# Kernel tuning notes

Measured on AMD Instinct MI355X. Metric: run time of the kernel, lower is better.

The kernel has to match this reference:

```python
import jax, jax.numpy as jnp
import numpy as np

B, K, D = 8, 4000, 256
H, DQ, DV = 8, 32, 32
WIN, PAD = 200, 50
STEP = WIN - 2 * PAD  # 100
BETA = 0.25


def setup_inputs() -> dict:
    key = jax.random.key(0)
    ks = jax.random.split(key, 14)
    s = 0.02
    return {
        "query": jax.random.normal(ks[0], (B, K, D), jnp.float32),
        "key": jax.random.normal(ks[1], (B, K, D), jnp.float32),
        "value": jax.random.normal(ks[2], (B, K, D), jnp.float32),
        "Wq": jax.random.normal(ks[3], (D, H * DQ), jnp.float32) * s,
        "bq": jax.random.normal(ks[4], (H * DQ,), jnp.float32) * s,
        "Wk": jax.random.normal(ks[5], (D, H * DQ), jnp.float32) * s,
        "bk": jax.random.normal(ks[6], (H * DQ,), jnp.float32) * s,
        "Wv": jax.random.normal(ks[7], (D, H * DV), jnp.float32) * s,
        "bv": jax.random.normal(ks[8], (H * DV,), jnp.float32) * s,
        "Wo": jax.random.normal(ks[9], (H * DV, D), jnp.float32) * s,
        "bo": jax.random.normal(ks[10], (D,), jnp.float32) * s,
    }


def _windows(x, n_win):
    starts = jnp.arange(n_win) * STEP
    idx = starts[:, None] + jnp.arange(WIN)[None, :]
    return x[:, :, idx, :]


def reference(query, key, value, Wq, bq, Wk, bk, Wv, bv, Wo, bo):
    b, k_len, d = query.shape
    pad = lambda t: jnp.pad(t, ((0, 0), (PAD, PAD), (0, 0)), mode='edge')  # replicate pad
    qp, kp, vp = pad(query), pad(key), pad(value)
    kpad = k_len + 2 * PAD
    n_win = (kpad - WIN) // STEP + 1

    def proj(x, Wm, bias, dh):
        y = x @ Wm + bias                       # [B, Kp, H*dh]
        return y.reshape(b, kpad, H, dh).transpose(0, 2, 1, 3)  # [B, H, Kp, dh]

    q = _windows(proj(qp, Wq, bq, DQ), n_win)
    kk = _windows(proj(kp, Wk, bk, DQ), n_win)
    v = _windows(proj(vp, Wv, bv, DV), n_win)

    scores = jnp.einsum('bhnid,bhnjd->bhnij', q, kk) / jnp.sqrt(jnp.float32(WIN))
    dist = jnp.abs(jnp.arange(WIN)[:, None] - jnp.arange(WIN)[None, :]).astype(scores.dtype)
    cauchy = (1.0 / (1.0 + BETA * dist * dist)) * (1.0 - jnp.eye(WIN, dtype=scores.dtype))
    scores = scores * cauchy
    causal = jnp.triu(jnp.ones((WIN, WIN), dtype=bool), k=1)  # attention_size is not None -> causal masking
    scores = jnp.where(causal, -jnp.inf, scores)
    attn = jax.nn.softmax(scores, axis=-1)
    out = jnp.einsum('bhnij,bhnjd->bhnid', attn, v)
    out = out[:, :, :, PAD:WIN - PAD, :].reshape(b, H, k_len, DV)
    out = out.transpose(0, 2, 1, 3).reshape(b, k_len, H * DV)  # heads concatenated, head-major slices
    return out @ Wo + bo
```

## Files before the change

kernel.cpp:

```cpp
#include <hip/hip_runtime.h>


typedef __bf16 bf16_t;
typedef __bf16 bf16x8 __attribute__((ext_vector_type(8)));
typedef float  f32x4  __attribute__((ext_vector_type(4)));

#define MFMA16(a, b, c) __builtin_amdgcn_mfma_f32_16x16x32_bf16((a), (b), (c), 0, 0, 0)

static __device__ __forceinline__ bf16x8 cvt8(float4 a, float4 b) {
  bf16x8 r;
  r[0] = (bf16_t)a.x; r[1] = (bf16_t)a.y; r[2] = (bf16_t)a.z; r[3] = (bf16_t)a.w;
  r[4] = (bf16_t)b.x; r[5] = (bf16_t)b.y; r[6] = (bf16_t)b.z; r[7] = (bf16_t)b.w;
  return r;
}

static __device__ __forceinline__ unsigned short bbits(bf16_t v) {
  union { bf16_t b; unsigned short u; } c; c.b = v; return c.u;
}

__global__ __launch_bounds__(256)
void prep_weights(const float* __restrict__ Wq, const float* __restrict__ Wk,
                  const float* __restrict__ Wv, const float* __restrict__ Wo,
                  bf16_t* __restrict__ wt) {
  const int mat  = blockIdx.x >> 6;
  const int tile = blockIdx.x & 63;
  const int kt = (tile >> 3) * 32, nt = (tile & 7) * 32;
  const float* W = (mat == 0) ? Wq : (mat == 1) ? Wk : (mat == 2) ? Wv : Wo;
  __shared__ float t[32][33];
  const int tx = threadIdx.x & 31, ty = threadIdx.x >> 5;
#pragma unroll
  for (int i = 0; i < 32; i += 8)
    t[ty + i][tx] = W[(size_t)(kt + ty + i) * 256 + nt + tx];
  __syncthreads();
  bf16_t* dst = wt + (size_t)mat * 65536;
#pragma unroll
  for (int i = 0; i < 32; i += 8)
    dst[(size_t)(nt + ty + i) * 256 + kt + tx] = (bf16_t)t[tx][ty + i];
}

static __device__ __forceinline__ void stage_B(const bf16_t* __restrict__ W,
                                               bf16_t* lb, int tid) {
#pragma unroll
  for (int i = 0; i < 16; ++i) {
    const int g    = tid + i * 512;
    const int row  = g >> 5;
    const int colb = (g & 31) << 4;
    const bf16x8 w = *(const bf16x8*)&W[row * 256 + (colb >> 1)];
    *(bf16x8*)((char*)lb + row * 512 + (colb ^ ((row & 7) << 4))) = w;
  }
}

__global__ __launch_bounds__(512)
void proj_gemm(const float* __restrict__ qx, const float* __restrict__ kx,
               const float* __restrict__ vx, const bf16_t* __restrict__ wt,
               const float* __restrict__ bq, const float* __restrict__ bk,
               const float* __restrict__ bv,
               bf16_t* __restrict__ qb, bf16_t* __restrict__ kb,
               bf16_t* __restrict__ vt, int M, float qscale) {
  const int mode = blockIdx.y;
  const float* X    = (mode == 0) ? qx : (mode == 1) ? kx : vx;
  const float* bias = (mode == 0) ? bq : (mode == 1) ? bk : bv;

  __shared__ bf16_t lb[65536];
  const int tid = threadIdx.x;
  stage_B(wt + (size_t)mode * 65536, lb, tid);

  const int lane = tid & 63, wv = tid >> 6;
  const int lo = lane & 15, hi = lane >> 4;
  const int m0 = blockIdx.x * 128;
  int ar = m0 + wv * 16 + lo; if (ar >= M) ar = M - 1;

  bf16x8 areg[8];
#pragma unroll
  for (int kk = 0; kk < 8; ++kk) {
    const float* ap = X + (size_t)ar * 256 + kk * 32 + hi * 8;
    areg[kk] = cvt8(((const float4*)ap)[0], ((const float4*)ap)[1]);
  }
  __syncthreads();

  f32x4 acc[16] = {};
#pragma unroll
  for (int kk = 0; kk < 8; ++kk) {
#pragma unroll
    for (int ni = 0; ni < 16; ++ni) {
      const int row = ni * 16 + lo;
      const int off = row * 512 + (((kk * 64) + hi * 16) ^ ((row & 7) << 4));
      const bf16x8 bfrag = *(const bf16x8*)((const char*)lb + off);
      acc[ni] = MFMA16(areg[kk], bfrag, acc[ni]);
    }
  }

  const int mb = m0 + wv * 16 + hi * 4;
  if (mb >= M) return;
#pragma unroll
  for (int ni = 0; ni < 16; ++ni) {
    const int n = ni * 16 + lo;
    const float bia = bias[n];
    if (mode == 0) {
#pragma unroll
      for (int r = 0; r < 4; ++r)
        qb[(size_t)(mb + r) * 256 + n] = (bf16_t)((acc[ni][r] + bia) * qscale);
    } else if (mode == 1) {
      const int b = mb / 4000, t = mb - b * 4000;
#pragma unroll
      for (int r = 0; r < 4; ++r)
        kb[((size_t)b * 4064 + t + 50 + r) * 256 + n] = (bf16_t)(acc[ni][r] + bia);
    } else {
      const int b = mb / 4000, t = mb - b * 4000;
      const int h = n >> 5, dv = n & 31;
      bf16_t* O = vt + ((size_t)((b * 8 + h) * 32 + dv)) * 4064 + t + 50;
      unsigned short e0 = bbits((bf16_t)(acc[ni][0] + bia));
      unsigned short e1 = bbits((bf16_t)(acc[ni][1] + bia));
      unsigned short e2 = bbits((bf16_t)(acc[ni][2] + bia));
      unsigned short e3 = bbits((bf16_t)(acc[ni][3] + bia));
      unsigned* O32 = (unsigned*)O;
      O32[0] = (unsigned)e0 | ((unsigned)e1 << 16);
      O32[1] = (unsigned)e2 | ((unsigned)e3 << 16);
    }
  }
}

__global__ __launch_bounds__(512)
void out_gemm(const bf16_t* __restrict__ ao, const bf16_t* __restrict__ wt,
              const float* __restrict__ bias, float* __restrict__ Out, int M) {
  __shared__ bf16_t lb[65536];
  const int tid = threadIdx.x;
  stage_B(wt, lb, tid);

  const int lane = tid & 63, wv = tid >> 6;
  const int lo = lane & 15, hi = lane >> 4;
  const int m0 = blockIdx.x * 128;
  int ar = m0 + wv * 16 + lo; if (ar >= M) ar = M - 1;

  bf16x8 areg[8];
#pragma unroll
  for (int kk = 0; kk < 8; ++kk)
    areg[kk] = *(const bf16x8*)&ao[(size_t)ar * 256 + kk * 32 + hi * 8];
  __syncthreads();

  f32x4 acc[16] = {};
#pragma unroll
  for (int kk = 0; kk < 8; ++kk) {
#pragma unroll
    for (int ni = 0; ni < 16; ++ni) {
      const int row = ni * 16 + lo;
      const int off = row * 512 + (((kk * 64) + hi * 16) ^ ((row & 7) << 4));
      const bf16x8 bfrag = *(const bf16x8*)((const char*)lb + off);
      acc[ni] = MFMA16(areg[kk], bfrag, acc[ni]);
    }
  }

  const int mb = m0 + wv * 16 + hi * 4;
  if (mb >= M) return;
#pragma unroll
  for (int ni = 0; ni < 16; ++ni) {
    const int n = ni * 16 + lo;
    const float bia = bias[n];
#pragma unroll
    for (int r = 0; r < 4; ++r)
      Out[(size_t)(mb + r) * 256 + n] = acc[ni][r] + bia;
  }
}

__global__ void fill_edges(bf16_t* __restrict__ kb, bf16_t* __restrict__ vt, int nb) {
  const int idx = blockIdx.x * 256 + threadIdx.x;
  const int kcnt = nb * 64 * 256;
  if (idx < kcnt) {
    const int b  = idx >> 14;
    const int pp = (idx >> 8) & 63;
    const int nn = idx & 255;
    const int p  = (pp < 50) ? pp : pp + 4000;
    bf16_t v = (pp < 50) ? kb[((size_t)b * 4064 + 50) * 256 + nn] : (bf16_t)0.f;
    kb[((size_t)b * 4064 + p) * 256 + nn] = v;
  } else {
    const int j  = idx - kcnt;
    const int bh = j >> 11;
    const int dv = (j >> 6) & 31;
    const int pp = j & 63;
    const int p  = (pp < 50) ? pp : pp + 4000;
    bf16_t v = (pp < 50) ? vt[((size_t)bh * 32 + dv) * 4064 + 50] : (bf16_t)0.f;
    vt[((size_t)bh * 32 + dv) * 4064 + p] = v;
  }
}

__global__ __launch_bounds__(448)
void attn_win(const bf16_t* __restrict__ qb, const bf16_t* __restrict__ kb,
              const bf16_t* __restrict__ vt, bf16_t* __restrict__ ao) {
  const int blk = blockIdx.x;
  const int n = blk % 40;
  const int h = (blk / 40) & 7;
  const int b = blk / 320;
  const int wv = threadIdx.x >> 6;
  const int lane = threadIdx.x & 63;
  const int lo = lane & 15, hi = lane >> 4;

  __shared__ __align__(16) bf16_t E[7][16][40];

  const int i0 = 50 + 16 * wv;
  int jtmax = (65 + 16 * wv) >> 4;
  if (jtmax > 9) jtmax = 9;
  const int reach = jtmax * 16 + 16;

  int tq = n * 100 + 16 * wv + lo;
  if (tq > 3999) tq = 3999;
  const bf16x8 qf = *(const bf16x8*)&qb[((size_t)b * 4000 + tq) * 256 + h * 32 + hi * 8];

  const f32x4 zero = {0.f, 0.f, 0.f, 0.f};
  bf16x8 onesf;
#pragma unroll
  for (int u = 0; u < 8; ++u) onesf[u] = (bf16_t)1.0f;

  f32x4 o0 = zero, o1 = zero, sm = zero;
  const size_t vbase = ((size_t)((b * 8 + h) * 32)) * 4064 + n * 100;
  const size_t kbase = ((size_t)(b * 4064 + n * 100)) * 256 + h * 32 + hi * 8;
  const int dbase = i0 + hi * 4 - lo;

#pragma unroll
  for (int kt = 0; kt < 5; ++kt) if (kt * 32 < reach) {
#pragma unroll
    for (int half = 0; half < 2; ++half) {
      const int jt = kt * 2 + half;
      if (jt <= jtmax) {
        const bf16x8 kf = *(const bf16x8*)&kb[kbase + (size_t)(jt * 16 + lo) * 256];
        const f32x4 s = MFMA16(qf, kf, zero);
#pragma unroll
        for (int r = 0; r < 4; ++r) {
          const int d = dbase + r - jt * 16;
          const float df = (float)d;
          float c = __builtin_amdgcn_rcpf(__builtin_fmaf(0.25f * df, df, 1.f));
          c = (d == 0) ? 0.f : c;
          float e = __expf(s[r] * c);
          e = (d < 0) ? 0.f : e;
          E[wv][hi * 4 + r][half * 16 + lo] = (bf16_t)e;
        }
      } else {
#pragma unroll
        for (int r = 0; r < 4; ++r)
          E[wv][hi * 4 + r][half * 16 + lo] = (bf16_t)0.f;
      }
    }
    const bf16x8 pf = *(const bf16x8*)&E[wv][lo][hi * 8];
    const bf16x8 v0 = *(const bf16x8*)&vt[vbase + (size_t)lo * 4064 + kt * 32 + hi * 8];
    const bf16x8 v1 = *(const bf16x8*)&vt[vbase + (size_t)(16 + lo) * 4064 + kt * 32 + hi * 8];
    o0 = MFMA16(pf, v0, o0);
    o1 = MFMA16(pf, v1, o1);
    sm = MFMA16(pf, onesf, sm);
  }

#pragma unroll
  for (int r = 0; r < 4; ++r) {
    const int i = i0 + hi * 4 + r;
    if (i < 150) {
      const float ri = __builtin_amdgcn_rcpf(sm[r]);
      const int t = n * 100 + i - 50;
      bf16_t* op = &ao[((size_t)b * 4000 + t) * 256 + h * 32];
      op[lo]      = (bf16_t)(o0[r] * ri);
      op[16 + lo] = (bf16_t)(o1[r] * ri);
    }
  }
}

extern "C" void kernel_launch(void* const* d_in, const int* in_sizes, int n_in,
                              void* d_out, int out_size, void* d_ws, size_t ws_size,
                              hipStream_t stream) {
  (void)in_sizes; (void)n_in; (void)out_size;
  const float* query = (const float*)d_in[0];
  const float* key   = (const float*)d_in[1];
  const float* value = (const float*)d_in[2];
  const float* Wq = (const float*)d_in[3];
  const float* bq = (const float*)d_in[4];
  const float* Wk = (const float*)d_in[5];
  const float* bk = (const float*)d_in[6];
  const float* Wv = (const float*)d_in[7];
  const float* bv = (const float*)d_in[8];
  const float* Wo = (const float*)d_in[9];
  const float* bo = (const float*)d_in[10];

  int bc = 8;
  while (bc > 1 && 524288ull + (unsigned long long)bc * 8257536ull > (unsigned long long)ws_size)
    bc >>= 1;

  bf16_t* wt = (bf16_t*)d_ws;
  bf16_t* qb = wt + 4 * 65536;
  bf16_t* kb = qb + (size_t)bc * 4000 * 256;
  bf16_t* vt = kb + (size_t)bc * 4064 * 256;
  bf16_t* ao = vt + (size_t)bc * 8 * 32 * 4064;

  prep_weights<<<256, 256, 0, stream>>>(Wq, Wk, Wv, Wo, wt);

  const float qscale = 0.07071067811865475f;

  for (int b0 = 0; b0 < 8; b0 += bc) {
    const int M = bc * 4000;
    const int mblk = (M + 127) / 128;
    const float* qx = query + (size_t)b0 * 4000 * 256;
    const float* kx = key   + (size_t)b0 * 4000 * 256;
    const float* vx = value + (size_t)b0 * 4000 * 256;
    float* ox = (float*)d_out + (size_t)b0 * 4000 * 256;

    proj_gemm<<<dim3(mblk, 3), 512, 0, stream>>>(qx, kx, vx, wt, bq, bk, bv,
                                                 qb, kb, vt, M, qscale);
    fill_edges<<<bc * 128, 256, 0, stream>>>(kb, vt, bc);
    attn_win<<<bc * 320, 448, 0, stream>>>(qb, kb, vt, ao);
    out_gemm<<<dim3(mblk), 512, 0, stream>>>(ao, wt + 3 * 65536, bo, ox, M);
  }
}
```

Measured before the change: 105.2 us.

## Retile projection and output GEMMs with K-looped small LDS tiles

Both GEMM kernels stop staging the whole 256x256 bf16 weight matrix (128KB) in shared memory per block. They now loop over K in chunks of 32, staging a 64-row activation tile and a 256x32 weight slice into padded LDS. Each of 4 waves computes a 64x64 output subtile. This cuts LDS use from 128KB to about 25KB per block, so several blocks can share a CU. In exchange there are more barriers and per-iteration global loads, and twice as many blocks.

After: 97.24 us. 1.08x faster.

```diff
diff --git a/kernel.cpp b/kernel.cpp
--- a/kernel.cpp
+++ b/kernel.cpp
@@ -38,19 +38,7 @@
     dst[(size_t)(nt + ty + i) * 256 + kt + tx] = (bf16_t)t[tx][ty + i];
 }
 
-static __device__ __forceinline__ void stage_B(const bf16_t* __restrict__ W,
-                                               bf16_t* lb, int tid) {
-#pragma unroll
-  for (int i = 0; i < 16; ++i) {
-    const int g    = tid + i * 512;
-    const int row  = g >> 5;
-    const int colb = (g & 31) << 4;
-    const bf16x8 w = *(const bf16x8*)&W[row * 256 + (colb >> 1)];
-    *(bf16x8*)((char*)lb + row * 512 + (colb ^ ((row & 7) << 4))) = w;
-  }
-}
-
-__global__ __launch_bounds__(512)
+__global__ __launch_bounds__(256)
 void proj_gemm(const float* __restrict__ qx, const float* __restrict__ kx,
                const float* __restrict__ vx, const bf16_t* __restrict__ wt,
                const float* __restrict__ bq, const float* __restrict__ bk,
@@ -60,105 +48,139 @@
   const int mode = blockIdx.y;
   const float* X    = (mode == 0) ? qx : (mode == 1) ? kx : vx;
   const float* bias = (mode == 0) ? bq : (mode == 1) ? bk : bv;
-
-  __shared__ bf16_t lb[65536];
-  const int tid = threadIdx.x;
-  stage_B(wt + (size_t)mode * 65536, lb, tid);
-
-  const int lane = tid & 63, wv = tid >> 6;
-  const int lo = lane & 15, hi = lane >> 4;
-  const int m0 = blockIdx.x * 128;
-  int ar = m0 + wv * 16 + lo; if (ar >= M) ar = M - 1;
-
-  bf16x8 areg[8];
-#pragma unroll
-  for (int kk = 0; kk < 8; ++kk) {
-    const float* ap = X + (size_t)ar * 256 + kk * 32 + hi * 8;
-    areg[kk] = cvt8(((const float4*)ap)[0], ((const float4*)ap)[1]);
-  }
-  __syncthreads();
-
-  f32x4 acc[16] = {};
-#pragma unroll
-  for (int kk = 0; kk < 8; ++kk) {
-#pragma unroll
-    for (int ni = 0; ni < 16; ++ni) {
-      const int row = ni * 16 + lo;
-      const int off = row * 512 + (((kk * 64) + hi * 16) ^ ((row & 7) << 4));
-      const bf16x8 bfrag = *(const bf16x8*)((const char*)lb + off);
-      acc[ni] = MFMA16(areg[kk], bfrag, acc[ni]);
-    }
-  }
-
-  const int mb = m0 + wv * 16 + hi * 4;
-  if (mb >= M) return;
-#pragma unroll
-  for (int ni = 0; ni < 16; ++ni) {
-    const int n = ni * 16 + lo;
-    const float bia = bias[n];
-    if (mode == 0) {
-#pragma unroll
-      for (int r = 0; r < 4; ++r)
-        qb[(size_t)(mb + r) * 256 + n] = (bf16_t)((acc[ni][r] + bia) * qscale);
-    } else if (mode == 1) {
-      const int b = mb / 4000, t = mb - b * 4000;
-#pragma unroll
-      for (int r = 0; r < 4; ++r)
-        kb[((size_t)b * 4064 + t + 50 + r) * 256 + n] = (bf16_t)(acc[ni][r] + bia);
-    } else {
-      const int b = mb / 4000, t = mb - b * 4000;
-      const int h = n >> 5, dv = n & 31;
-      bf16_t* O = vt + ((size_t)((b * 8 + h) * 32 + dv)) * 4064 + t + 50;
-      unsigned short e0 = bbits((bf16_t)(acc[ni][0] + bia));
-      unsigned short e1 = bbits((bf16_t)(acc[ni][1] + bia));
-      unsigned short e2 = bbits((bf16_t)(acc[ni][2] + bia));
-      unsigned short e3 = bbits((bf16_t)(acc[ni][3] + bia));
-      unsigned* O32 = (unsigned*)O;
-      O32[0] = (unsigned)e0 | ((unsigned)e1 << 16);
-      O32[1] = (unsigned)e2 | ((unsigned)e3 << 16);
-    }
-  }
-}
-
-__global__ __launch_bounds__(512)
+  const bf16_t* W   = wt + (size_t)mode * 65536;
+
+  __shared__ bf16_t la[64 * 40];
+  __shared__ bf16_t lb[256 * 40];
+  const int tid  = threadIdx.x;
+  const int lane = tid & 63;
+  const int wv   = tid >> 6;
+  const int lo   = lane & 15, hi = lane >> 4;
+  const int m0   = blockIdx.x * 64;
+  int ar = m0 + (tid >> 2); if (ar >= M) ar = M - 1;
+  const int acg  = (tid & 3) * 8;
+  const int brow = tid >> 2;
+  const int bcg  = (tid & 3) * 8;
+
+  f32x4 acc[4][4] = {};
+
+  for (int kk = 0; kk < 256; kk += 32) {
+    {
+      const float* ap = X + (size_t)ar * 256 + kk + acg;
+      *(bf16x8*)&la[(tid >> 2) * 40 + acg] =
+          cvt8(((const float4*)ap)[0], ((const float4*)ap)[1]);
+    }
+#pragma unroll
+    for (int rr = 0; rr < 4; ++rr) {
+      const int row = brow + rr * 64;
+      *(bf16x8*)&lb[row * 40 + bcg] =
+          *(const bf16x8*)&W[(size_t)row * 256 + kk + bcg];
+    }
+    __syncthreads();
+
+    bf16x8 af[4], bfv[4];
+#pragma unroll
+    for (int mi = 0; mi < 4; ++mi)
+      af[mi] = *(const bf16x8*)&la[(mi * 16 + lo) * 40 + hi * 8];
+#pragma unroll
+    for (int ni = 0; ni < 4; ++ni)
+      bfv[ni] = *(const bf16x8*)&lb[(wv * 64 + ni * 16 + lo) * 40 + hi * 8];
+#pragma unroll
+    for (int mi = 0; mi < 4; ++mi)
+#pragma unroll
+      for (int ni = 0; ni < 4; ++ni)
+        acc[mi][ni] = MFMA16(af[mi], bfv[ni], acc[mi][ni]);
+    __syncthreads();
+  }
+
+#pragma unroll
+  for (int mi = 0; mi < 4; ++mi) {
+    const int mb = m0 + mi * 16 + hi * 4;
+    if (mb >= M) continue;
+#pragma unroll
+    for (int ni = 0; ni < 4; ++ni) {
+      const int n = wv * 64 + ni * 16 + lo;
+      const float bia = bias[n];
+      if (mode == 0) {
+#pragma unroll
+        for (int r = 0; r < 4; ++r)
+          qb[(size_t)(mb + r) * 256 + n] = (bf16_t)((acc[mi][ni][r] + bia) * qscale);
+      } else if (mode == 1) {
+        const int b = mb / 4000, t = mb - b * 4000;
+#pragma unroll
+        for (int r = 0; r < 4; ++r)
+          kb[((size_t)b * 4064 + t + 50 + r) * 256 + n] = (bf16_t)(acc[mi][ni][r] + bia);
+      } else {
+        const int b = mb / 4000, t = mb - b * 4000;
+        const int h = n >> 5, dv = n & 31;
+        bf16_t* O = vt + ((size_t)((b * 8 + h) * 32 + dv)) * 4064 + t + 50;
+        unsigned short e0 = bbits((bf16_t)(acc[mi][ni][0] + bia));
+        unsigned short e1 = bbits((bf16_t)(acc[mi][ni][1] + bia));
+        unsigned short e2 = bbits((bf16_t)(acc[mi][ni][2] + bia));
+        unsigned short e3 = bbits((bf16_t)(acc[mi][ni][3] + bia));
+        unsigned* O32 = (unsigned*)O;
+        O32[0] = (unsigned)e0 | ((unsigned)e1 << 16);
+        O32[1] = (unsigned)e2 | ((unsigned)e3 << 16);
+      }
+    }
+  }
+}
+
+__global__ __launch_bounds__(256)
 void out_gemm(const bf16_t* __restrict__ ao, const bf16_t* __restrict__ wt,
               const float* __restrict__ bias, float* __restrict__ Out, int M) {
-  __shared__ bf16_t lb[65536];
-  const int tid = threadIdx.x;
-  stage_B(wt, lb, tid);
-
-  const int lane = tid & 63, wv = tid >> 6;
-  const int lo = lane & 15, hi = lane >> 4;
-  const int m0 = blockIdx.x * 128;
-  int ar = m0 + wv * 16 + lo; if (ar >= M) ar = M - 1;
-
-  bf16x8 areg[8];
-#pragma unroll
-  for (int kk = 0; kk < 8; ++kk)
-    areg[kk] = *(const bf16x8*)&ao[(size_t)ar * 256 + kk * 32 + hi * 8];
-  __syncthreads();
-
-  f32x4 acc[16] = {};
-#pragma unroll
-  for (int kk = 0; kk < 8; ++kk) {
-#pragma unroll
-    for (int ni = 0; ni < 16; ++ni) {
-      const int row = ni * 16 + lo;
-      const int off = row * 512 + (((kk * 64) + hi * 16) ^ ((row & 7) << 4));
-      const bf16x8 bfrag = *(const bf16x8*)((const char*)lb + off);
-      acc[ni] = MFMA16(areg[kk], bfrag, acc[ni]);
-    }
-  }
-
-  const int mb = m0 + wv * 16 + hi * 4;
-  if (mb >= M) return;
-#pragma unroll
-  for (int ni = 0; ni < 16; ++ni) {
-    const int n = ni * 16 + lo;
-    const float bia = bias[n];
-#pragma unroll
-    for (int r = 0; r < 4; ++r)
-      Out[(size_t)(mb + r) * 256 + n] = acc[ni][r] + bia;
+  __shared__ bf16_t la[64 * 40];
+  __shared__ bf16_t lb[256 * 40];
+  const int tid  = threadIdx.x;
+  const int lane = tid & 63;
+  const int wv   = tid >> 6;
+  const int lo   = lane & 15, hi = lane >> 4;
+  const int m0   = blockIdx.x * 64;
+  int ar = m0 + (tid >> 2); if (ar >= M) ar = M - 1;
+  const int acg  = (tid & 3) * 8;
+  const int brow = tid >> 2;
+  const int bcg  = (tid & 3) * 8;
+
+  f32x4 acc[4][4] = {};
+
+  for (int kk = 0; kk < 256; kk += 32) {
+    *(bf16x8*)&la[(tid >> 2) * 40 + acg] =
+        *(const bf16x8*)&ao[(size_t)ar * 256 + kk + acg];
+#pragma unroll
+    for (int rr = 0; rr < 4; ++rr) {
+      const int row = brow + rr * 64;
+      *(bf16x8*)&lb[row * 40 + bcg] =
+          *(const bf16x8*)&wt[(size_t)row * 256 + kk + bcg];
+    }
+    __syncthreads();
+
+    bf16x8 af[4], bfv[4];
+#pragma unroll
+    for (int mi = 0; mi < 4; ++mi)
+      af[mi] = *(const bf16x8*)&la[(mi * 16 + lo) * 40 + hi * 8];
+#pragma unroll
+    for (int ni = 0; ni < 4; ++ni)
+      bfv[ni] = *(const bf16x8*)&lb[(wv * 64 + ni * 16 + lo) * 40 + hi * 8];
+#pragma unroll
+    for (int mi = 0; mi < 4; ++mi)
+#pragma unroll
+      for (int ni = 0; ni < 4; ++ni)
+        acc[mi][ni] = MFMA16(af[mi], bfv[ni], acc[mi][ni]);
+    __syncthreads();
+  }
+
+#pragma unroll
+  for (int mi = 0; mi < 4; ++mi) {
+    const int mb = m0 + mi * 16 + hi * 4;
+    if (mb >= M) continue;
+#pragma unroll
+    for (int ni = 0; ni < 4; ++ni) {
+      const int n = wv * 64 + ni * 16 + lo;
+      const float bia = bias[n];
+#pragma unroll
+      for (int r = 0; r < 4; ++r)
+        Out[(size_t)(mb + r) * 256 + n] = acc[mi][ni][r] + bia;
+    }
   }
 }
 
@@ -292,16 +314,16 @@
 
   for (int b0 = 0; b0 < 8; b0 += bc) {
     const int M = bc * 4000;
-    const int mblk = (M + 127) / 128;
+    const int mblk = (M + 63) / 64;
     const float* qx = query + (size_t)b0 * 4000 * 256;
     const float* kx = key   + (size_t)b0 * 4000 * 256;
     const float* vx = value + (size_t)b0 * 4000 * 256;
     float* ox = (float*)d_out + (size_t)b0 * 4000 * 256;
 
-    proj_gemm<<<dim3(mblk, 3), 512, 0, stream>>>(qx, kx, vx, wt, bq, bk, bv,
+    proj_gemm<<<dim3(mblk, 3), 256, 0, stream>>>(qx, kx, vx, wt, bq, bk, bv,
                                                  qb, kb, vt, M, qscale);
     fill_edges<<<bc * 128, 256, 0, stream>>>(kb, vt, bc);
     attn_win<<<bc * 320, 448, 0, stream>>>(qb, kb, vt, ao);
-    out_gemm<<<dim3(mblk), 512, 0, stream>>>(ao, wt + 3 * 65536, bo, ox, M);
-  }
-}
+    out_gemm<<<dim3(mblk), 256, 0, stream>>>(ao, wt + 3 * 65536, bo, ox, M);
+  }
+}
```
